# Optimization experiments

Measured on AMD Instinct MI355X. Metric: run time of the kernel, lower is better.

The kernel has to match this reference:

```python
import jax, jax.numpy as jnp
import numpy as np

# Dimensions (from DKVB defaults)
B, N = 4, 64            # batch, tokens
D = 2048                # embedding_dim (dim_embed)
C = 256                 # num_codebooks (heads, separate codebook per head)
E = 128                 # projection_embedding_dim == codebook_dim
M = 4096                # codes_per_codebook (codebook_size)
V = 10                  # dim_memory (value dim)


def setup_inputs() -> dict:
    key = jax.random.key(0)
    k1, k2, k3, k4 = jax.random.split(key, 4)
    xavier_std = (2.0 / (D + E)) ** 0.5  # nn.init.xavier_normal_ on [C, D, E]
    return {
        "embeddings": jax.random.normal(k1, (B, N, D), jnp.float32),
        "rand_proj": jax.random.normal(k2, (C, D, E), jnp.float32) * xavier_std,
        "codebook": jax.random.normal(k3, (C, M, E), jnp.float32),
        "values": jax.random.normal(k4, (C, M, V), jnp.float32),
    }


def reference(embeddings, rand_proj, codebook, values):
    # 1) random projection per codebook: 'b n d, c d e -> b n c e'
    xp = jnp.einsum('bnd,cde->bnce', embeddings, rand_proj)  # [B,N,C,E]
    # 2) per-codebook nearest neighbor (Euclidean): argmin ||x - e||^2
    dots = jnp.einsum('bnce,cme->bncm', xp, codebook)        # [B,N,C,M]
    x_sq = jnp.sum(xp * xp, axis=-1)                          # [B,N,C]
    e_sq = jnp.sum(codebook * codebook, axis=-1)              # [C,M]
    d2 = x_sq[..., None] - 2.0 * dots + e_sq[None, None]      # [B,N,C,M]
    idx = jnp.argmin(d2, axis=-1)                             # [B,N,C] int
    # 3) gather learned memory values per codebook, then average pool over codebooks
    mem = values[jnp.arange(C)[None, None, :], idx]           # [B,N,C,V]
    return jnp.mean(mem, axis=2)                              # [B,N,V]
```

## Files before the change

### kernel.cpp

```cpp
#include <hip/hip_runtime.h>

#define BN 256
#define D  2048
#define C  256
#define E  128
#define M  4096
#define V  10

__global__ __launch_bounds__(256) void k1_xp(const float* __restrict__ emb,
                                             const float* __restrict__ proj,
                                             float* __restrict__ xp) {
  const int c   = blockIdx.y;
  const int bn0 = blockIdx.x * 128;
  const int tid = threadIdx.x;
  const int ty  = tid >> 4;
  const int tx  = tid & 15;

  __shared__ __align__(16) float As[32][128];
  __shared__ __align__(16) float Bs[32][128];

  float acc[8][8];
#pragma unroll
  for (int i = 0; i < 8; ++i)
#pragma unroll
    for (int j = 0; j < 8; ++j) acc[i][j] = 0.0f;

  const int srow = tid >> 1;
  const int skof = (tid & 1) * 16;
  const int brow = tid >> 3;
  const int beof = (tid & 7) * 16;

  const float* embp  = emb + (size_t)(bn0 + srow) * D + skof;
  const float* projp = proj + (size_t)c * D * E + (size_t)brow * E + beof;

  for (int k0 = 0; k0 < D; k0 += 32) {
    __syncthreads();
#pragma unroll
    for (int q = 0; q < 4; ++q) {
      float4 va = *(const float4*)(embp + k0 + q * 4);
      As[skof + q * 4 + 0][srow] = va.x;
      As[skof + q * 4 + 1][srow] = va.y;
      As[skof + q * 4 + 2][srow] = va.z;
      As[skof + q * 4 + 3][srow] = va.w;
    }
#pragma unroll
    for (int q = 0; q < 4; ++q) {
      *(float4*)&Bs[brow][beof + q * 4] =
          *(const float4*)(projp + (size_t)k0 * E + q * 4);
    }
    __syncthreads();
#pragma unroll
    for (int k = 0; k < 32; ++k) {
      float a[8], b[8];
      *(float4*)&a[0] = *(const float4*)&As[k][ty * 8];
      *(float4*)&a[4] = *(const float4*)&As[k][ty * 8 + 4];
      *(float4*)&b[0] = *(const float4*)&Bs[k][tx * 8];
      *(float4*)&b[4] = *(const float4*)&Bs[k][tx * 8 + 4];
#pragma unroll
      for (int i = 0; i < 8; ++i)
#pragma unroll
        for (int j = 0; j < 8; ++j) acc[i][j] = fmaf(a[i], b[j], acc[i][j]);
    }
  }

#pragma unroll
  for (int i = 0; i < 8; ++i) {
    float* op = xp + ((size_t)c * BN + bn0 + ty * 8 + i) * E + tx * 8;
    *(float4*)op       = make_float4(acc[i][0], acc[i][1], acc[i][2], acc[i][3]);
    *(float4*)(op + 4) = make_float4(acc[i][4], acc[i][5], acc[i][6], acc[i][7]);
  }
}

__global__ __launch_bounds__(256) void k2_argmin(const float* __restrict__ xp,
                                                 const float* __restrict__ cb,
                                                 int* __restrict__ idxo) {
  const int c   = blockIdx.y;
  const int bn0 = blockIdx.x * 64;
  const int tid = threadIdx.x;
  const int ty  = tid >> 4;
  const int tx  = tid & 15;

  __shared__ __align__(16) float As[128][64];
  __shared__ __align__(16) float Bs[64][64];
  __shared__ float esqp[64][4];

  {
    const int row = tid >> 2;
    const int eof = (tid & 3) * 32;
    const float* p = xp + ((size_t)c * BN + bn0 + row) * E + eof;
#pragma unroll
    for (int q = 0; q < 8; ++q) {
      float4 v = *(const float4*)(p + q * 4);
      As[eof + q * 4 + 0][row] = v.x;
      As[eof + q * 4 + 1][row] = v.y;
      As[eof + q * 4 + 2][row] = v.z;
      As[eof + q * 4 + 3][row] = v.w;
    }
  }

  float bestv[4];
  int   besti[4];
#pragma unroll
  for (int i = 0; i < 4; ++i) { bestv[i] = 3.4e38f; besti[i] = 0; }

  const int sm   = tid >> 2;
  const int sq   = tid & 3;
  const int seof = sq * 16;

  for (int mt = 0; mt < M / 64; ++mt) {
    float acc[4][4];
#pragma unroll
    for (int i = 0; i < 4; ++i)
#pragma unroll
      for (int j = 0; j < 4; ++j) acc[i][j] = 0.0f;
    float esqa = 0.0f;

    const float* cbp = cb + ((size_t)c * M + mt * 64 + sm) * E + seof;

    __syncthreads();
#pragma unroll
    for (int q = 0; q < 4; ++q) {
      float4 v = *(const float4*)(cbp + q * 4);
      esqa = fmaf(v.x, v.x, esqa); esqa = fmaf(v.y, v.y, esqa);
      esqa = fmaf(v.z, v.z, esqa); esqa = fmaf(v.w, v.w, esqa);
      Bs[seof + q * 4 + 0][sm] = v.x;
      Bs[seof + q * 4 + 1][sm] = v.y;
      Bs[seof + q * 4 + 2][sm] = v.z;
      Bs[seof + q * 4 + 3][sm] = v.w;
    }
    __syncthreads();
#pragma unroll
    for (int k = 0; k < 64; ++k) {
      float a[4], b[4];
      *(float4*)a = *(const float4*)&As[k][ty * 4];
      *(float4*)b = *(const float4*)&Bs[k][tx * 4];
#pragma unroll
      for (int i = 0; i < 4; ++i)
#pragma unroll
        for (int j = 0; j < 4; ++j) acc[i][j] = fmaf(a[i], b[j], acc[i][j]);
    }
    __syncthreads();
#pragma unroll
    for (int q = 0; q < 4; ++q) {
      float4 v = *(const float4*)(cbp + 64 + q * 4);
      esqa = fmaf(v.x, v.x, esqa); esqa = fmaf(v.y, v.y, esqa);
      esqa = fmaf(v.z, v.z, esqa); esqa = fmaf(v.w, v.w, esqa);
      Bs[seof + q * 4 + 0][sm] = v.x;
      Bs[seof + q * 4 + 1][sm] = v.y;
      Bs[seof + q * 4 + 2][sm] = v.z;
      Bs[seof + q * 4 + 3][sm] = v.w;
    }
    esqp[sm][sq] = esqa;
    __syncthreads();
#pragma unroll
    for (int k = 0; k < 64; ++k) {
      float a[4], b[4];
      *(float4*)a = *(const float4*)&As[64 + k][ty * 4];
      *(float4*)b = *(const float4*)&Bs[k][tx * 4];
#pragma unroll
      for (int i = 0; i < 4; ++i)
#pragma unroll
        for (int j = 0; j < 4; ++j) acc[i][j] = fmaf(a[i], b[j], acc[i][j]);
    }
#pragma unroll
    for (int j = 0; j < 4; ++j) {
      const int col = tx * 4 + j;
      const float es = esqp[col][0] + esqp[col][1] + esqp[col][2] + esqp[col][3];
      const int mg = mt * 64 + col;
#pragma unroll
      for (int i = 0; i < 4; ++i) {
        float s = fmaf(-2.0f, acc[i][j], es);
        if (s < bestv[i]) { bestv[i] = s; besti[i] = mg; }
      }
    }
  }

  __syncthreads();
  float* redv = &As[0][0];
  int*   redi = (int*)&As[32][0];
#pragma unroll
  for (int i = 0; i < 4; ++i) {
    redv[(ty * 4 + i) * 16 + tx] = bestv[i];
    redi[(ty * 4 + i) * 16 + tx] = besti[i];
  }
  __syncthreads();
  if (tid < 64) {
    float bv = 3.4e38f; int bi = 0x7fffffff;
    for (int x = 0; x < 16; ++x) {
      float v = redv[tid * 16 + x];
      int   id = redi[tid * 16 + x];
      if (v < bv || (v == bv && id < bi)) { bv = v; bi = id; }
    }
    idxo[c * BN + bn0 + tid] = bi;
  }
}

__global__ __launch_bounds__(256) void k3_gather(const int* __restrict__ idxw,
                                                 const float* __restrict__ vals,
                                                 float* __restrict__ out) {
  const int bn = blockIdx.x;
  const int t  = threadIdx.x;
  __shared__ float red[256][V];
  const int id = idxw[t * BN + bn];
  const float* vp = vals + ((size_t)t * M + id) * V;
#pragma unroll
  for (int j = 0; j < V; ++j) red[t][j] = vp[j];
  __syncthreads();
  for (int s = 128; s > 0; s >>= 1) {
    if (t < s) {
#pragma unroll
      for (int j = 0; j < V; ++j) red[t][j] += red[t + s][j];
    }
    __syncthreads();
  }
  if (t < V) out[bn * V + t] = red[0][t] * (1.0f / 256.0f);
}

extern "C" void kernel_launch(void* const* d_in, const int* in_sizes, int n_in,
                              void* d_out, int out_size, void* d_ws, size_t ws_size,
                              hipStream_t stream) {
  const float* emb  = (const float*)d_in[0];
  const float* proj = (const float*)d_in[1];
  const float* cb   = (const float*)d_in[2];
  const float* vals = (const float*)d_in[3];
  float* out = (float*)d_out;

  float* xp   = (float*)d_ws;
  int*   idxw = (int*)((char*)d_ws + (size_t)C * BN * E * 4);

  k1_xp    <<<dim3(2, C), 256, 0, stream>>>(emb, proj, xp);
  k2_argmin<<<dim3(4, C), 256, 0, stream>>>(xp, cb, idxw);
  k3_gather<<<BN, 256, 0, stream>>>(idxw, vals, out);
}
```

Measured before the change: 2.094 ms.

## Register-prefetch global tiles and double-buffer LDS in projection and argmin kernels

The projection GEMM kernel now double-buffers its LDS tiles and prefetches the next K-slice into registers, so global loads overlap the FMA loop and one barrier per step is dropped. The argmin kernel is restructured to use 128-code tiles loaded in 32-wide K chunks. It also prefetches the next codebook chunk into registers during compute and uses a 4x8 per-thread microtile. This is meant to hide global memory latency and raise arithmetic intensity, at the cost of more registers and LDS.

```diff
diff --git a/kernel.cpp b/kernel.cpp
--- a/kernel.cpp
+++ b/kernel.cpp
@@ -16,8 +16,8 @@
   const int ty  = tid >> 4;
   const int tx  = tid & 15;
 
-  __shared__ __align__(16) float As[32][128];
-  __shared__ __align__(16) float Bs[32][128];
+  __shared__ __align__(16) float As[2][32][128];
+  __shared__ __align__(16) float Bs[2][32][128];
 
   float acc[8][8];
 #pragma unroll
@@ -33,35 +33,50 @@
   const float* embp  = emb + (size_t)(bn0 + srow) * D + skof;
   const float* projp = proj + (size_t)c * D * E + (size_t)brow * E + beof;
 
-  for (int k0 = 0; k0 < D; k0 += 32) {
-    __syncthreads();
-#pragma unroll
-    for (int q = 0; q < 4; ++q) {
-      float4 va = *(const float4*)(embp + k0 + q * 4);
-      As[skof + q * 4 + 0][srow] = va.x;
-      As[skof + q * 4 + 1][srow] = va.y;
-      As[skof + q * 4 + 2][srow] = va.z;
-      As[skof + q * 4 + 3][srow] = va.w;
-    }
-#pragma unroll
-    for (int q = 0; q < 4; ++q) {
-      *(float4*)&Bs[brow][beof + q * 4] =
-          *(const float4*)(projp + (size_t)k0 * E + q * 4);
-    }
-    __syncthreads();
-#pragma unroll
-    for (int k = 0; k < 32; ++k) {
-      float a[8], b[8];
-      *(float4*)&a[0] = *(const float4*)&As[k][ty * 8];
-      *(float4*)&a[4] = *(const float4*)&As[k][ty * 8 + 4];
-      *(float4*)&b[0] = *(const float4*)&Bs[k][tx * 8];
-      *(float4*)&b[4] = *(const float4*)&Bs[k][tx * 8 + 4];
-#pragma unroll
-      for (int i = 0; i < 8; ++i)
-#pragma unroll
-        for (int j = 0; j < 8; ++j) acc[i][j] = fmaf(a[i], b[j], acc[i][j]);
-    }
-  }
+  float4 ra[4], rb[4];
+#pragma unroll
+  for (int q = 0; q < 4; ++q) {
+    ra[q] = *(const float4*)(embp + q * 4);
+    rb[q] = *(const float4*)(projp + q * 4);
+  }
+
+#define K1_STEP(BUF, KK)                                                      \
+  {                                                                           \
+    _Pragma("unroll")                                                         \
+    for (int q = 0; q < 4; ++q) {                                             \
+      As[BUF][skof + q * 4 + 0][srow] = ra[q].x;                              \
+      As[BUF][skof + q * 4 + 1][srow] = ra[q].y;                              \
+      As[BUF][skof + q * 4 + 2][srow] = ra[q].z;                              \
+      As[BUF][skof + q * 4 + 3][srow] = ra[q].w;                              \
+      *(float4*)&Bs[BUF][brow][beof + q * 4] = rb[q];                         \
+    }                                                                         \
+    __syncthreads();                                                          \
+    if ((KK) + 32 < D) {                                                      \
+      _Pragma("unroll")                                                       \
+      for (int q = 0; q < 4; ++q) {                                           \
+        ra[q] = *(const float4*)(embp + (KK) + 32 + q * 4);                   \
+        rb[q] = *(const float4*)(projp + (size_t)((KK) + 32) * E + q * 4);    \
+      }                                                                       \
+    }                                                                         \
+    _Pragma("unroll")                                                         \
+    for (int k = 0; k < 32; ++k) {                                            \
+      float a[8], b[8];                                                       \
+      *(float4*)&a[0] = *(const float4*)&As[BUF][k][ty * 8];                  \
+      *(float4*)&a[4] = *(const float4*)&As[BUF][k][ty * 8 + 4];              \
+      *(float4*)&b[0] = *(const float4*)&Bs[BUF][k][tx * 8];                  \
+      *(float4*)&b[4] = *(const float4*)&Bs[BUF][k][tx * 8 + 4];              \
+      _Pragma("unroll")                                                       \
+      for (int i = 0; i < 8; ++i)                                             \
+        _Pragma("unroll")                                                     \
+        for (int j = 0; j < 8; ++j) acc[i][j] = fmaf(a[i], b[j], acc[i][j]);  \
+    }                                                                         \
+  }
+
+  for (int k0 = 0; k0 < D; k0 += 64) {
+    K1_STEP(0, k0)
+    K1_STEP(1, k0 + 32)
+  }
+#undef K1_STEP
 
 #pragma unroll
   for (int i = 0; i < 8; ++i) {
@@ -81,8 +96,8 @@
   const int tx  = tid & 15;
 
   __shared__ __align__(16) float As[128][64];
-  __shared__ __align__(16) float Bs[64][64];
-  __shared__ float esqp[64][4];
+  __shared__ __align__(16) float Bs[32][128];
+  __shared__ float esqp[128][2];
 
   {
     const int row = tid >> 2;
@@ -103,70 +118,62 @@
 #pragma unroll
   for (int i = 0; i < 4; ++i) { bestv[i] = 3.4e38f; besti[i] = 0; }
 
-  const int sm   = tid >> 2;
-  const int sq   = tid & 3;
-  const int seof = sq * 16;
-
-  for (int mt = 0; mt < M / 64; ++mt) {
-    float acc[4][4];
+  const int sm  = tid >> 1;
+  const int par = tid & 1;
+  const float* cbp = cb + ((size_t)c * M + sm) * E + par * 16;
+
+  float4 rb[4];
+#pragma unroll
+  for (int q = 0; q < 4; ++q) rb[q] = *(const float4*)(cbp + q * 4);
+
+  for (int mt = 0; mt < M / 128; ++mt) {
+    float acc[4][8];
 #pragma unroll
     for (int i = 0; i < 4; ++i)
 #pragma unroll
-      for (int j = 0; j < 4; ++j) acc[i][j] = 0.0f;
+      for (int j = 0; j < 8; ++j) acc[i][j] = 0.0f;
     float esqa = 0.0f;
 
-    const float* cbp = cb + ((size_t)c * M + mt * 64 + sm) * E + seof;
-
-    __syncthreads();
-#pragma unroll
-    for (int q = 0; q < 4; ++q) {
-      float4 v = *(const float4*)(cbp + q * 4);
-      esqa = fmaf(v.x, v.x, esqa); esqa = fmaf(v.y, v.y, esqa);
-      esqa = fmaf(v.z, v.z, esqa); esqa = fmaf(v.w, v.w, esqa);
-      Bs[seof + q * 4 + 0][sm] = v.x;
-      Bs[seof + q * 4 + 1][sm] = v.y;
-      Bs[seof + q * 4 + 2][sm] = v.z;
-      Bs[seof + q * 4 + 3][sm] = v.w;
-    }
-    __syncthreads();
-#pragma unroll
-    for (int k = 0; k < 64; ++k) {
-      float a[4], b[4];
-      *(float4*)a = *(const float4*)&As[k][ty * 4];
-      *(float4*)b = *(const float4*)&Bs[k][tx * 4];
-#pragma unroll
-      for (int i = 0; i < 4; ++i)
-#pragma unroll
-        for (int j = 0; j < 4; ++j) acc[i][j] = fmaf(a[i], b[j], acc[i][j]);
-    }
-    __syncthreads();
-#pragma unroll
-    for (int q = 0; q < 4; ++q) {
-      float4 v = *(const float4*)(cbp + 64 + q * 4);
-      esqa = fmaf(v.x, v.x, esqa); esqa = fmaf(v.y, v.y, esqa);
-      esqa = fmaf(v.z, v.z, esqa); esqa = fmaf(v.w, v.w, esqa);
-      Bs[seof + q * 4 + 0][sm] = v.x;
-      Bs[seof + q * 4 + 1][sm] = v.y;
-      Bs[seof + q * 4 + 2][sm] = v.z;
-      Bs[seof + q * 4 + 3][sm] = v.w;
-    }
-    esqp[sm][sq] = esqa;
-    __syncthreads();
-#pragma unroll
-    for (int k = 0; k < 64; ++k) {
-      float a[4], b[4];
-      *(float4*)a = *(const float4*)&As[64 + k][ty * 4];
-      *(float4*)b = *(const float4*)&Bs[k][tx * 4];
-#pragma unroll
-      for (int i = 0; i < 4; ++i)
-#pragma unroll
-        for (int j = 0; j < 4; ++j) acc[i][j] = fmaf(a[i], b[j], acc[i][j]);
-    }
-#pragma unroll
-    for (int j = 0; j < 4; ++j) {
-      const int col = tx * 4 + j;
-      const float es = esqp[col][0] + esqp[col][1] + esqp[col][2] + esqp[col][3];
-      const int mg = mt * 64 + col;
+    for (int kc = 0; kc < 4; ++kc) {
+      __syncthreads();
+#pragma unroll
+      for (int q = 0; q < 4; ++q) {
+        float4 v = rb[q];
+        esqa = fmaf(v.x, v.x, esqa); esqa = fmaf(v.y, v.y, esqa);
+        esqa = fmaf(v.z, v.z, esqa); esqa = fmaf(v.w, v.w, esqa);
+        Bs[par * 16 + q * 4 + 0][sm] = v.x;
+        Bs[par * 16 + q * 4 + 1][sm] = v.y;
+        Bs[par * 16 + q * 4 + 2][sm] = v.z;
+        Bs[par * 16 + q * 4 + 3][sm] = v.w;
+      }
+      if (kc == 3) esqp[sm][par] = esqa;
+      __syncthreads();
+      {
+        const int t = mt * 4 + kc + 1;
+        if (t < (M / 128) * 4) {
+          const float* p = cbp + (size_t)(t >> 2) * (128 * E) + (t & 3) * 32;
+#pragma unroll
+          for (int q = 0; q < 4; ++q) rb[q] = *(const float4*)(p + q * 4);
+        }
+      }
+      const int kb = kc * 32;
+#pragma unroll
+      for (int k = 0; k < 32; ++k) {
+        float a[4], b[8];
+        *(float4*)&a[0] = *(const float4*)&As[kb + k][ty * 4];
+        *(float4*)&b[0] = *(const float4*)&Bs[k][tx * 8];
+        *(float4*)&b[4] = *(const float4*)&Bs[k][tx * 8 + 4];
+#pragma unroll
+        for (int i = 0; i < 4; ++i)
+#pragma unroll
+          for (int j = 0; j < 8; ++j) acc[i][j] = fmaf(a[i], b[j], acc[i][j]);
+      }
+    }
+#pragma unroll
+    for (int j = 0; j < 8; ++j) {
+      const int col = tx * 8 + j;
+      const float es = esqp[col][0] + esqp[col][1];
+      const int mg = mt * 128 + col;
 #pragma unroll
       for (int i = 0; i < 4; ++i) {
         float s = fmaf(-2.0f, acc[i][j], es);
```

After: 3.004 ms. 43.4% more time.
